# Kernel tuning notes

Measured on AMD Instinct MI355X. Metric: run time of the kernel, lower is better.

Reference implementation:

```python
import jax, jax.numpy as jnp
import numpy as np
from jax import lax

EPS = 1e-5
K = 7
G = 4


def _dwconv_bn(x, w, g, b, m, v):
    # depthwise 3x3, pad 1, then BN (eval mode with running stats)
    C = x.shape[1]
    y = lax.conv_general_dilated(x, w, (1, 1), [(1, 1), (1, 1)],
                                 feature_group_count=C,
                                 dimension_numbers=('NCHW', 'OIHW', 'NCHW'))
    scale = (g / jnp.sqrt(v + EPS))[None, :, None, None]
    return (y - m[None, :, None, None]) * scale + b[None, :, None, None]


def _proj(t, pw1, pb1, pw2, pb2):
    # 1x1 conv -> GELU(exact) -> 1x1 conv, on small spatial maps
    h = jnp.einsum('bchw,oc->bohw', t, pw1) + pb1[None, :, None, None]
    h = jax.nn.gelu(h, approximate=False)
    return jnp.einsum('bchw,oc->bohw', h, pw2) + pb2[None, :, None, None]


def setup_inputs() -> dict:
    key = jax.random.key(0)
    ks = jax.random.split(key, 17)
    B, C, H, W = 16, 256, 56, 56
    r = C // 4
    inp = {
        'x1': jax.random.normal(ks[0], (B, C, H, W), jnp.float32),
        'dw1_w': jax.random.normal(ks[1], (C, 1, 3, 3), jnp.float32) * 0.1,
        'dw1_g': jax.random.uniform(ks[2], (C,), jnp.float32, 0.5, 1.5),
        'dw1_b': jax.random.normal(ks[3], (C,), jnp.float32) * 0.1,
        'dw1_m': jax.random.normal(ks[4], (C,), jnp.float32) * 0.1,
        'dw1_v': jax.random.uniform(ks[5], (C,), jnp.float32, 0.5, 1.5),
        'dw2_w': jax.random.normal(ks[6], (C, 1, 3, 3), jnp.float32) * 0.1,
        'dw2_g': jax.random.uniform(ks[7], (C,), jnp.float32, 0.5, 1.5),
        'dw2_b': jax.random.normal(ks[8], (C,), jnp.float32) * 0.1,
        'dw2_m': jax.random.normal(ks[9], (C,), jnp.float32) * 0.1,
        'dw2_v': jax.random.uniform(ks[10], (C,), jnp.float32, 0.5, 1.5),
        'weight1': jax.random.normal(ks[11], (G, C, K, K), jnp.float32) * 0.02,
        'bias1': jax.random.normal(ks[12], (G, C), jnp.float32) * 0.02,
        'pw1': jax.random.normal(ks[13], (r, C), jnp.float32) * 0.05,
        'pb1': jax.random.normal(ks[14], (r,), jnp.float32) * 0.05,
        'pw2': jax.random.normal(ks[15], (C * G, r), jnp.float32) * 0.05,
        'pb2': jax.random.normal(ks[16], (C * G,), jnp.float32) * 0.05,
    }
    return inp


def reference(x1, dw1_w, dw1_g, dw1_b, dw1_m, dw1_v,
              dw2_w, dw2_g, dw2_b, dw2_m, dw2_v,
              weight1, bias1, pw1, pb1, pw2, pb2):
    B, C, H, W = x1.shape
    # gated fuse: relu6(dw1(x)) * dw2(x)
    a = jnp.clip(_dwconv_bn(x1, dw1_w, dw1_g, dw1_b, dw1_m, dw1_v), 0.0, 6.0)
    x_fuse = a * _dwconv_bn(x1, dw2_w, dw2_g, dw2_b, dw2_m, dw2_v)

    # adaptive avg pool to (K,K): H,W multiples of K -> uniform block means
    pooled = x_fuse.reshape(B, C, K, H // K, K, W // K).mean(axis=(3, 5))

    # dynamic kernel: proj -> softmax over groups -> weighted sum of weight1
    scale1 = _proj(pooled, pw1, pb1, pw2, pb2).reshape(B, G, C, K, K)
    scale1 = jax.nn.softmax(scale1, axis=1)
    w_dyn = jnp.sum(scale1 * weight1[None], axis=1)  # [B, C, K, K]

    # dynamic bias
    mean_x = x_fuse.mean(axis=(-2, -1), keepdims=True)  # [B, C, 1, 1]
    sb = _proj(mean_x, pw1, pb1, pw2, pb2).reshape(B, G, C)
    sb = jax.nn.softmax(sb, axis=1)
    b_dyn = jnp.sum(sb * bias1[None], axis=1)  # [B, C]

    # per-sample depthwise conv with dynamic weights
    pad = K // 2

    def per_sample(xi, wi):  # xi [C,H,W], wi [C,K,K]
        y = lax.conv_general_dilated(xi[None], wi[:, None], (1, 1),
                                     [(pad, pad), (pad, pad)],
                                     feature_group_count=C,
                                     dimension_numbers=('NCHW', 'OIHW', 'NCHW'))
        return y[0]

    out = jax.vmap(per_sample)(x_fuse, w_dyn)  # [B, C, H, W]
    return out + b_dyn[:, :, None, None]
```

## Files before the change

### kernel.cpp

```cpp
#include <hip/hip_runtime.h>
#include <math.h>

#define BATCH 16
#define CH 256
#define HW 56
#define NPIX (HW*HW)
#define KK 7

#define S1 64
__global__ __launch_bounds__(256) void k1_fuse(
    const float* __restrict__ x1,
    const float* __restrict__ dw1w, const float* __restrict__ g1, const float* __restrict__ b1,
    const float* __restrict__ m1, const float* __restrict__ v1,
    const float* __restrict__ dw2w, const float* __restrict__ g2, const float* __restrict__ b2,
    const float* __restrict__ m2, const float* __restrict__ v2,
    float* __restrict__ xf,
    float* __restrict__ pooled)
{
    const int bc = blockIdx.x;
    const int c  = bc & 255;
    const int t  = threadIdx.x;

    __shared__ __attribute__((aligned(16))) float halo[58*S1];
    __shared__ float part[196];

    {
        float4 z = make_float4(0.f, 0.f, 0.f, 0.f);
        float4* h4 = (float4*)halo;
        for (int i = t; i < 58*S1/4; i += 256) h4[i] = z;
    }

    float w1[9], w2[9];
    #pragma unroll
    for (int k = 0; k < 9; k++) { w1[k] = dw1w[c*9+k]; w2[k] = dw2w[c*9+k]; }
    const float sc1 = g1[c] * rsqrtf(v1[c] + 1e-5f);
    const float be1 = b1[c] - m1[c] * sc1;
    const float sc2 = g2[c] * rsqrtf(v2[c] + 1e-5f);
    const float be2 = b2[c] - m2[c] * sc2;
    __syncthreads();

    const float4* xp4 = (const float4*)(x1 + (size_t)bc * NPIX);
    if (t < 196) {
        float4 v[4];
        #pragma unroll
        for (int q = 0; q < 4; q++) v[q] = xp4[q*196 + t];
        #pragma unroll
        for (int q = 0; q < 4; q++) {
            int p = (q*196 + t) * 4;
            int i = p / 56, j = p - i * 56;
            *(float4*)&halo[(i+1)*S1 + 4 + j] = v[q];
        }
    }
    __syncthreads();

    float tile_sum = 0.f;
    if (t < 196) {
        const int ty = t / 14, tx = t - ty * 14;
        float y1a[4][4], y2a[4][4];
        #pragma unroll
        for (int a = 0; a < 4; a++)
            #pragma unroll
            for (int e = 0; e < 4; e++) { y1a[a][e] = 0.f; y2a[a][e] = 0.f; }

        #pragma unroll
        for (int iy = 0; iy < 6; iy++) {
            const float* hr = &halo[(4*ty + iy)*S1 + 4*tx];
            float4 a4 = *(const float4*)hr;
            float4 b4 = *(const float4*)(hr + 4);
            float  c1 = hr[8];
            float rb[9];
            rb[0]=a4.x; rb[1]=a4.y; rb[2]=a4.z; rb[3]=a4.w;
            rb[4]=b4.x; rb[5]=b4.y; rb[6]=b4.z; rb[7]=b4.w; rb[8]=c1;
            #pragma unroll
            for (int tyy = 0; tyy < 4; tyy++) {
                const int ky = iy - tyy;
                if (ky >= 0 && ky < 3) {
                    #pragma unroll
                    for (int e = 0; e < 4; e++)
                        #pragma unroll
                        for (int dj = 0; dj < 3; dj++) {
                            float xv = rb[3 + e + dj];
                            y1a[tyy][e] += xv * w1[ky*3+dj];
                            y2a[tyy][e] += xv * w2[ky*3+dj];
                        }
                }
            }
        }
        float* plane = xf + (size_t)bc * NPIX;
        #pragma unroll
        for (int tyy = 0; tyy < 4; tyy++) {
            float res[4];
            #pragma unroll
            for (int e = 0; e < 4; e++) {
                float y1 = y1a[tyy][e] * sc1 + be1;
                float y2 = y2a[tyy][e] * sc2 + be2;
                float a = fminf(fmaxf(y1, 0.f), 6.f);
                res[e] = a * y2;
                tile_sum += res[e];
            }
            float4 r4; r4.x=res[0]; r4.y=res[1]; r4.z=res[2]; r4.w=res[3];
            *(float4*)(plane + (4*ty + tyy)*56 + 4*tx) = r4;
        }
        part[t] = tile_sum;
    }
    __syncthreads();
    if (t < 49) {
        int ph = t / 7, pw = t - ph * 7;
        float s = part[(2*ph  )*14 + 2*pw] + part[(2*ph  )*14 + 2*pw + 1]
                + part[(2*ph+1)*14 + 2*pw] + part[(2*ph+1)*14 + 2*pw + 1];
        pooled[(size_t)bc * 49 + t] = s * (1.f/64.f);
    }
}

__global__ __launch_bounds__(256) void k2a(
    const float* __restrict__ pooled, const float* __restrict__ pw1,
    const float* __restrict__ pb1, float* __restrict__ h)
{
    const int b  = blockIdx.x;
    const int oc = blockIdx.y;
    const int t  = threadIdx.x;
    __shared__ float pl[256*50];

    const float* pp = pooled + (size_t)b * 256 * 49;
    for (int idx = t; idx < 256*49; idx += 256) {
        int cc = idx / 49, p = idx - cc * 49;
        pl[cc*50 + p] = pp[idx];
    }
    __syncthreads();
    {
        float s = 0.f;
        #pragma unroll
        for (int p = 0; p < 49; p++) s += pl[t*50 + p];
        pl[t*50 + 49] = s * (1.f/49.f);
    }
    __syncthreads();

    for (int idx = t; idx < 16*50; idx += 256) {
        int ol = idx / 50, p = idx - ol * 50;
        int o = oc * 16 + ol;
        const float* wrow = pw1 + o * 256;
        float acc = pb1[o];
        #pragma unroll 8
        for (int cc = 0; cc < 256; cc++) acc += wrow[cc] * pl[cc*50 + p];
        float gv = 0.5f * acc * (1.f + erff(acc * 0.70710678118654752f));
        h[((size_t)b * 50 + p) * 64 + o] = gv;
    }
}

__global__ __launch_bounds__(256) void k2b(
    const float* __restrict__ h, const float* __restrict__ pw2, const float* __restrict__ pb2,
    const float* __restrict__ weight1, const float* __restrict__ bias1,
    float* __restrict__ w_dyn, float* __restrict__ b_dyn)
{
    const int b   = blockIdx.x;
    const int cch = blockIdx.y;
    const int t   = threadIdx.x;
    const int c_base = cch * 16;

    __shared__ __attribute__((aligned(16))) float hl[50*64];
    __shared__ float sl[64*51];

    const float* hp = h + (size_t)b * 50 * 64;
    for (int i = t; i < 800; i += 256) ((float4*)hl)[i] = ((const float4*)hp)[i];

    const int row = t & 63;
    const int pb  = t >> 6;
    const int g   = row >> 4, cl = row & 15;
    const int o2  = (g << 8) + c_base + cl;

    float wreg[64];
    {
        const float4* w4 = (const float4*)(pw2 + (size_t)o2 * 64);
        #pragma unroll
        for (int r4 = 0; r4 < 16; r4++) {
            float4 v = w4[r4];
            wreg[4*r4] = v.x; wreg[4*r4+1] = v.y; wreg[4*r4+2] = v.z; wreg[4*r4+3] = v.w;
        }
    }
    const float bias2 = pb2[o2];
    __syncthreads();

    for (int p = pb; p < 50; p += 4) {
        const float4* hv = (const float4*)&hl[p*64];
        float acc = bias2;
        #pragma unroll
        for (int r4 = 0; r4 < 16; r4++) {
            float4 v = hv[r4];
            acc += wreg[4*r4]*v.x + wreg[4*r4+1]*v.y + wreg[4*r4+2]*v.z + wreg[4*r4+3]*v.w;
        }
        sl[row*51 + p] = acc;
    }
    __syncthreads();

    for (int idx = t; idx < 16*50; idx += 256) {
        int cl2 = idx / 50, p = idx - cl2 * 50;
        float s0 = sl[(cl2     )*51 + p];
        float s1 = sl[(16 + cl2)*51 + p];
        float s2 = sl[(32 + cl2)*51 + p];
        float s3 = sl[(48 + cl2)*51 + p];
        float mx = fmaxf(fmaxf(s0, s1), fmaxf(s2, s3));
        float e0 = expf(s0-mx), e1 = expf(s1-mx), e2 = expf(s2-mx), e3 = expf(s3-mx);
        float inv = 1.f / (e0+e1+e2+e3);
        e0 *= inv; e1 *= inv; e2 *= inv; e3 *= inv;
        int cc = c_base + cl2;
        if (p < 49) {
            float wv = e0*weight1[(0*256+cc)*49+p] + e1*weight1[(1*256+cc)*49+p]
                     + e2*weight1[(2*256+cc)*49+p] + e3*weight1[(3*256+cc)*49+p];
            w_dyn[((size_t)b*256 + cc)*49 + p] = wv;
        } else {
            b_dyn[b*256 + cc] = e0*bias1[cc] + e1*bias1[256+cc] + e2*bias1[512+cc] + e3*bias1[768+cc];
        }
    }
}

#define S3 68
__global__ __launch_bounds__(256) void k3_dyn(
    const float* __restrict__ w_dyn, const float* __restrict__ b_dyn,
    float* __restrict__ io)
{
    const int bc = blockIdx.x;
    const int t  = threadIdx.x;
    __shared__ __attribute__((aligned(16))) float halo[62*S3];

    {
        float4 z = make_float4(0.f, 0.f, 0.f, 0.f);
        float4* h4 = (float4*)halo;
        for (int i = t; i < 62*S3/4; i += 256) h4[i] = z;
    }

    float w[49];
    const float* wp = w_dyn + (size_t)bc * 49;
    #pragma unroll
    for (int k = 0; k < 49; k++) w[k] = wp[k];
    const float bias = b_dyn[bc];
    __syncthreads();

    float* plane = io + (size_t)bc * NPIX;
    const float4* pl4 = (const float4*)plane;
    if (t < 196) {
        float4 v[4];
        #pragma unroll
        for (int q = 0; q < 4; q++) v[q] = pl4[q*196 + t];
        #pragma unroll
        for (int q = 0; q < 4; q++) {
            int p = (q*196 + t) * 4;
            int i = p / 56, j = p - i * 56;
            *(float4*)&halo[(i+3)*S3 + 4 + j] = v[q];
        }
    }
    __syncthreads();

    if (t < 196) {
        const int ty = t / 14, tx = t - ty * 14;
        const int oy = ty * 4, ox = tx * 4;
        float acc[4][4];
        #pragma unroll
        for (int a = 0; a < 4; a++)
            #pragma unroll
            for (int bb = 0; bb < 4; bb++) acc[a][bb] = bias;

        #pragma unroll
        for (int iy = 0; iy < 10; iy++) {
            const float* hr = &halo[(oy+iy)*S3 + ox];
            float4 a = *(const float4*)hr;
            float4 b = *(const float4*)(hr + 4);
            float4 c = *(const float4*)(hr + 8);
            float row[12];
            row[0]=a.x; row[1]=a.y; row[2]=a.z; row[3]=a.w;
            row[4]=b.x; row[5]=b.y; row[6]=b.z; row[7]=b.w;
            row[8]=c.x; row[9]=c.y; row[10]=c.z; row[11]=c.w;
            #pragma unroll
            for (int tyy = 0; tyy < 4; tyy++) {
                const int ky = iy - tyy;
                if (ky >= 0 && ky < 7) {
                    #pragma unroll
                    for (int txx = 0; txx < 4; txx++)
                        #pragma unroll
                        for (int kx = 0; kx < 7; kx++)
                            acc[tyy][txx] += row[1+txx+kx] * w[ky*7+kx];
                }
            }
        }
        #pragma unroll
        for (int tyy = 0; tyy < 4; tyy++) {
            float4 r4; r4.x = acc[tyy][0]; r4.y = acc[tyy][1]; r4.z = acc[tyy][2]; r4.w = acc[tyy][3];
            *(float4*)(plane + (oy+tyy)*56 + ox) = r4;
        }
    }
}

extern "C" void kernel_launch(void* const* d_in, const int* in_sizes, int n_in,
                              void* d_out, int out_size, void* d_ws, size_t ws_size,
                              hipStream_t stream) {
    const float* x1    = (const float*)d_in[0];
    const float* dw1w  = (const float*)d_in[1];
    const float* dw1g  = (const float*)d_in[2];
    const float* dw1b  = (const float*)d_in[3];
    const float* dw1m  = (const float*)d_in[4];
    const float* dw1v  = (const float*)d_in[5];
    const float* dw2w  = (const float*)d_in[6];
    const float* dw2g  = (const float*)d_in[7];
    const float* dw2b  = (const float*)d_in[8];
    const float* dw2m  = (const float*)d_in[9];
    const float* dw2v  = (const float*)d_in[10];
    const float* weight1 = (const float*)d_in[11];
    const float* bias1   = (const float*)d_in[12];
    const float* pw1     = (const float*)d_in[13];
    const float* pb1     = (const float*)d_in[14];
    const float* pw2     = (const float*)d_in[15];
    const float* pb2     = (const float*)d_in[16];

    float* out = (float*)d_out;
    float* ws  = (float*)d_ws;
    float* pooled = ws;
    float* h      = ws + 200704;
    float* w_dyn  = ws + 251904;
    float* b_dyn  = ws + 452608;

    k1_fuse<<<BATCH*CH, 256, 0, stream>>>(x1, dw1w, dw1g, dw1b, dw1m, dw1v,
                                          dw2w, dw2g, dw2b, dw2m, dw2v, out, pooled);
    k2a<<<dim3(BATCH, 4), 256, 0, stream>>>(pooled, pw1, pb1, h);
    k2b<<<dim3(BATCH, 16), 256, 0, stream>>>(h, pw2, pb2, weight1, bias1, w_dyn, b_dyn);
    k3_dyn<<<BATCH*CH, 256, 0, stream>>>(w_dyn, b_dyn, out);
}
```

Measured before the change: 203.6 us.

## Drop shared halo in fuse kernel, read neighbors from global, separate xfuse buffer

The first kernel no longer stages the input plane in shared memory. Each thread loads its 3x3 neighborhood of float4 tiles straight from global memory, zeroing out-of-bounds values, and uses launch bounds of (256,4). The fused map now goes to a separate workspace buffer instead of the output, so the dynamic-conv kernel reads xfuse and writes out, and it issues its global loads before zeroing the halo. This removes the LDS zero-fill, staging and barriers, in exchange for redundant global/L2 reads of overlapping tiles and an extra 51 MB workspace buffer.

```diff
diff --git a/kernel.cpp b/kernel.cpp
--- a/kernel.cpp
+++ b/kernel.cpp
@@ -7,8 +7,7 @@
 #define NPIX (HW*HW)
 #define KK 7
 
-#define S1 64
-__global__ __launch_bounds__(256) void k1_fuse(
+__global__ __launch_bounds__(256, 4) void k1_fuse(
     const float* __restrict__ x1,
     const float* __restrict__ dw1w, const float* __restrict__ g1, const float* __restrict__ b1,
     const float* __restrict__ m1, const float* __restrict__ v1,
@@ -21,14 +20,7 @@
     const int c  = bc & 255;
     const int t  = threadIdx.x;
 
-    __shared__ __attribute__((aligned(16))) float halo[58*S1];
     __shared__ float part[196];
-
-    {
-        float4 z = make_float4(0.f, 0.f, 0.f, 0.f);
-        float4* h4 = (float4*)halo;
-        for (int i = t; i < 58*S1/4; i += 256) h4[i] = z;
-    }
 
     float w1[9], w2[9];
     #pragma unroll
@@ -37,25 +29,13 @@
     const float be1 = b1[c] - m1[c] * sc1;
     const float sc2 = g2[c] * rsqrtf(v2[c] + 1e-5f);
     const float be2 = b2[c] - m2[c] * sc2;
-    __syncthreads();
-
-    const float4* xp4 = (const float4*)(x1 + (size_t)bc * NPIX);
-    if (t < 196) {
-        float4 v[4];
-        #pragma unroll
-        for (int q = 0; q < 4; q++) v[q] = xp4[q*196 + t];
-        #pragma unroll
-        for (int q = 0; q < 4; q++) {
-            int p = (q*196 + t) * 4;
-            int i = p / 56, j = p - i * 56;
-            *(float4*)&halo[(i+1)*S1 + 4 + j] = v[q];
-        }
-    }
-    __syncthreads();
-
-    float tile_sum = 0.f;
-    if (t < 196) {
-        const int ty = t / 14, tx = t - ty * 14;
+
+    const int ty = t / 14, tx = t - ty * 14;
+    const float* plane = x1 + (size_t)bc * NPIX;
+
+    float res[4][4];
+    if (t < 196) {
+        const int oy = 4 * ty;
         float y1a[4][4], y2a[4][4];
         #pragma unroll
         for (int a = 0; a < 4; a++)
@@ -64,13 +44,22 @@
 
         #pragma unroll
         for (int iy = 0; iy < 6; iy++) {
-            const float* hr = &halo[(4*ty + iy)*S1 + 4*tx];
-            float4 a4 = *(const float4*)hr;
-            float4 b4 = *(const float4*)(hr + 4);
-            float  c1 = hr[8];
-            float rb[9];
-            rb[0]=a4.x; rb[1]=a4.y; rb[2]=a4.z; rb[3]=a4.w;
-            rb[4]=b4.x; rb[5]=b4.y; rb[6]=b4.z; rb[7]=b4.w; rb[8]=c1;
+            const int r   = oy - 1 + iy;
+            const bool rok = (r >= 0) && (r < 56);
+            const int rc  = rok ? r : 0;
+            float rb[12];
+            #pragma unroll
+            for (int k = 0; k < 3; k++) {
+                const int cx  = tx - 1 + k;
+                const bool cv = (cx >= 0) && (cx < 14);
+                const int cc2 = cv ? cx : 0;
+                const bool ok = rok && cv;
+                float4 v = *(const float4*)(plane + rc*56 + 4*cc2);
+                rb[4*k+0] = ok ? v.x : 0.f;
+                rb[4*k+1] = ok ? v.y : 0.f;
+                rb[4*k+2] = ok ? v.z : 0.f;
+                rb[4*k+3] = ok ? v.w : 0.f;
+            }
             #pragma unroll
             for (int tyy = 0; tyy < 4; tyy++) {
                 const int ky = iy - tyy;
@@ -86,21 +75,17 @@
                 }
             }
         }
-        float* plane = xf + (size_t)bc * NPIX;
-        #pragma unroll
-        for (int tyy = 0; tyy < 4; tyy++) {
-            float res[4];
+        float tile_sum = 0.f;
+        #pragma unroll
+        for (int tyy = 0; tyy < 4; tyy++)
             #pragma unroll
             for (int e = 0; e < 4; e++) {
                 float y1 = y1a[tyy][e] * sc1 + be1;
                 float y2 = y2a[tyy][e] * sc2 + be2;
                 float a = fminf(fmaxf(y1, 0.f), 6.f);
-                res[e] = a * y2;
-                tile_sum += res[e];
+                res[tyy][e] = a * y2;
+                tile_sum += res[tyy][e];
             }
-            float4 r4; r4.x=res[0]; r4.y=res[1]; r4.z=res[2]; r4.w=res[3];
-            *(float4*)(plane + (4*ty + tyy)*56 + 4*tx) = r4;
-        }
         part[t] = tile_sum;
     }
     __syncthreads();
@@ -109,6 +94,14 @@
         float s = part[(2*ph  )*14 + 2*pw] + part[(2*ph  )*14 + 2*pw + 1]
                 + part[(2*ph+1)*14 + 2*pw] + part[(2*ph+1)*14 + 2*pw + 1];
         pooled[(size_t)bc * 49 + t] = s * (1.f/64.f);
+    }
+    if (t < 196) {
+        float* op = xf + (size_t)bc * NPIX;
+        #pragma unroll
+        for (int tyy = 0; tyy < 4; tyy++) {
+            float4 r4; r4.x=res[tyy][0]; r4.y=res[tyy][1]; r4.z=res[tyy][2]; r4.w=res[tyy][3];
+            *(float4*)(op + (4*ty + tyy)*56 + 4*tx) = r4;
+        }
     }
 }
 
@@ -215,12 +208,20 @@
 
 #define S3 68
 __global__ __launch_bounds__(256) void k3_dyn(
+    const float* __restrict__ xf,
     const float* __restrict__ w_dyn, const float* __restrict__ b_dyn,
-    float* __restrict__ io)
+    float* __restrict__ out)
 {
     const int bc = blockIdx.x;
     const int t  = threadIdx.x;
     __shared__ __attribute__((aligned(16))) float halo[62*S3];
+
+    const float4* pl4 = (const float4*)(xf + (size_t)bc * NPIX);
+    float4 v[4];
+    if (t < 196) {
+        #pragma unroll
+        for (int q = 0; q < 4; q++) v[q] = pl4[q*196 + t];
+    }
 
     {
         float4 z = make_float4(0.f, 0.f, 0.f, 0.f);
@@ -235,12 +236,7 @@
     const float bias = b_dyn[bc];
     __syncthreads();
 
-    float* plane = io + (size_t)bc * NPIX;
-    const float4* pl4 = (const float4*)plane;
-    if (t < 196) {
-        float4 v[4];
-        #pragma unroll
-        for (int q = 0; q < 4; q++) v[q] = pl4[q*196 + t];
+    if (t < 196) {
         #pragma unroll
         for (int q = 0; q < 4; q++) {
             int p = (q*196 + t) * 4;
@@ -281,10 +277,11 @@
                 }
             }
         }
+        float* op = out + (size_t)bc * NPIX;
         #pragma unroll
         for (int tyy = 0; tyy < 4; tyy++) {
             float4 r4; r4.x = acc[tyy][0]; r4.y = acc[tyy][1]; r4.z = acc[tyy][2]; r4.w = acc[tyy][3];
-            *(float4*)(plane + (oy+tyy)*56 + ox) = r4;
+            *(float4*)(op + (oy+tyy)*56 + ox) = r4;
         }
     }
 }
@@ -312,14 +309,15 @@
 
     float* out = (float*)d_out;
     float* ws  = (float*)d_ws;
-    float* pooled = ws;
-    float* h      = ws + 200704;
-    float* w_dyn  = ws + 251904;
-    float* b_dyn  = ws + 452608;
+    float* xfuse  = ws;
+    float* pooled = ws + 12845056;
+    float* h      = ws + 13045760;
+    float* w_dyn  = ws + 13096960;
+    float* b_dyn  = ws + 13297664;
 
     k1_fuse<<<BATCH*CH, 256, 0, stream>>>(x1, dw1w, dw1g, dw1b, dw1m, dw1v,
-                                          dw2w, dw2g, dw2b, dw2m, dw2v, out, pooled);
+                                          dw2w, dw2g, dw2b, dw2m, dw2v, xfuse, pooled);
     k2a<<<dim3(BATCH, 4), 256, 0, stream>>>(pooled, pw1, pb1, h);
     k2b<<<dim3(BATCH, 16), 256, 0, stream>>>(h, pw2, pb2, weight1, bias1, w_dyn, b_dyn);
-    k3_dyn<<<BATCH*CH, 256, 0, stream>>>(w_dyn, b_dyn, out);
-}
+    k3_dyn<<<BATCH*CH, 256, 0, stream>>>(xfuse, w_dyn, b_dyn, out);
+}
```

After: 215.9 us. 1.06x slower.
